# Performance work log

Measured on AMD Instinct MI355X. Metric: run time of the kernel, lower is better.

Reference implementation:

```python
import jax, jax.numpy as jnp
import numpy as np

VOCAB, HIDDEN = 32000, 512
BATCH, SEQLEN = 256, 128


def setup_inputs() -> dict:
    key = jax.random.key(0)
    k1, k2, k3, k4, k5 = jax.random.split(key, 5)
    bound = 1.0 / np.sqrt(HIDDEN)  # PyTorch RNNCell init scale
    return {
        "input": jax.random.randint(k1, (BATCH, SEQLEN), 0, VOCAB, dtype=jnp.int64),
        "hidden": jnp.zeros((BATCH, HIDDEN), dtype=jnp.float32),
        "emb_table": jax.random.normal(k2, (VOCAB, HIDDEN), dtype=jnp.float32),
        "W_ih": jax.random.uniform(k3, (HIDDEN, HIDDEN), jnp.float32, -bound, bound),
        "W_hh": jax.random.uniform(k4, (HIDDEN, HIDDEN), jnp.float32, -bound, bound),
        "b_ih": jax.random.uniform(k5, (HIDDEN,), jnp.float32, -bound, bound),
        "b_hh": jax.random.uniform(jax.random.fold_in(key, 9), (HIDDEN,), jnp.float32, -bound, bound),
    }


def reference(input, hidden, emb_table, W_ih, W_hh, b_ih, b_hh):
    # embedded: [B, T, H]
    embedded = emb_table[input]
    # Precompute the input projection for all timesteps in one GEMM: [B, T, H]
    x_proj = jnp.einsum("bth,ih->bti", embedded, W_ih) + b_ih

    def step(h, x_t):
        # PyTorch RNNCell: h' = tanh(x W_ih^T + b_ih + h W_hh^T + b_hh)
        h_new = jnp.tanh(x_t + h @ W_hh.T + b_hh)
        return h_new, h_new

    h_final, outs = jax.lax.scan(step, hidden, jnp.swapaxes(x_proj, 0, 1))
    outputs = jnp.swapaxes(outs, 0, 1)  # [B, T, H]
    return outputs, h_final
```

## Files before the change

kernel.cpp:

```cpp
#include <hip/hip_runtime.h>
#include <cstdint>

#define VOCAB   32000
#define HIDDEN  512
#define BATCH   256
#define SEQLEN  128

typedef _Float16 f16;
typedef _Float16 f16x2 __attribute__((ext_vector_type(2)));
typedef _Float16 f16x4 __attribute__((ext_vector_type(4)));
typedef _Float16 f16x8 __attribute__((ext_vector_type(8)));
typedef float    f32x4 __attribute__((ext_vector_type(4)));


__global__ __launch_bounds__(256) void conv_f16_kernel(
    const float* __restrict__ emb, const float* __restrict__ wih,
    const float* __restrict__ whh, f16* __restrict__ emb16,
    f16* __restrict__ wih16, f16* __restrict__ whh16)
{
  const long long EMB_N = (long long)VOCAB * HIDDEN;
  const long long W_N   = (long long)HIDDEN * HIDDEN;
  long long idx = ((long long)blockIdx.x * blockDim.x + threadIdx.x) * 4;
  const float* src; f16* dst; long long off;
  if (idx < EMB_N)            { src = emb; dst = emb16; off = idx; }
  else if (idx < EMB_N + W_N) { src = wih; dst = wih16; off = idx - EMB_N; }
  else                        { src = whh; dst = whh16; off = idx - EMB_N - W_N; }
  float4 v = *(const float4*)(src + off);
  f16x4 o = { (f16)v.x, (f16)v.y, (f16)v.z, (f16)v.w };
  *(f16x4*)(dst + off) = o;
}

__global__ __launch_bounds__(256) void xproj_kernel(
    const int*   __restrict__ tokens,
    const f16*   __restrict__ emb16,
    const f16*   __restrict__ wih16,
    const float* __restrict__ b_ih,
    float*       __restrict__ out)
{
  const int lane = threadIdx.x & 63;
  const int wave = threadIdx.x >> 6;
  const int m0 = blockIdx.y * 128 + (wave >> 1) * 64;
  const int n0 = blockIdx.x * 128 + (wave & 1) * 64;
  const int lr = lane & 15;
  const int lg = lane >> 4;

  const f16* aptr[4];
  const f16* bptr[4];
#pragma unroll
  for (int mi = 0; mi < 4; ++mi) {
    int row = m0 + mi * 16 + lr;
    int tok = tokens[row];
    aptr[mi] = emb16 + (long long)tok * HIDDEN;
  }
#pragma unroll
  for (int ni = 0; ni < 4; ++ni) {
    int col = n0 + ni * 16 + lr;
    bptr[ni] = wih16 + (long long)col * HIDDEN;
  }

  f32x4 acc[4][4];
#pragma unroll
  for (int ni = 0; ni < 4; ++ni) {
    float b = b_ih[n0 + ni * 16 + lr];
#pragma unroll
    for (int mi = 0; mi < 4; ++mi) acc[mi][ni] = (f32x4){b, b, b, b};
  }

  for (int kt = 0; kt < 16; ++kt) {
    const int kb = kt * 32 + lg * 8;
    f16x8 af[4], bf[4];
#pragma unroll
    for (int mi = 0; mi < 4; ++mi) af[mi] = *(const f16x8*)(aptr[mi] + kb);
#pragma unroll
    for (int ni = 0; ni < 4; ++ni) bf[ni] = *(const f16x8*)(bptr[ni] + kb);
#pragma unroll
    for (int mi = 0; mi < 4; ++mi)
#pragma unroll
      for (int ni = 0; ni < 4; ++ni)
        acc[mi][ni] = __builtin_amdgcn_mfma_f32_16x16x32_f16(
            af[mi], bf[ni], acc[mi][ni], 0, 0, 0);
  }

#pragma unroll
  for (int mi = 0; mi < 4; ++mi)
#pragma unroll
    for (int ni = 0; ni < 4; ++ni)
#pragma unroll
      for (int j = 0; j < 4; ++j) {
        int rg = m0 + mi * 16 + lg * 4 + j;
        int cg = n0 + ni * 16 + lr;
        out[(long long)rg * HIDDEN + cg] = acc[mi][ni][j];
      }
}

__device__ __forceinline__ float dp2(uint32_t w, uint32_t h, float acc) {
  f16x2 wv = __builtin_bit_cast(f16x2, w);
  f16x2 hv = __builtin_bit_cast(f16x2, h);
#if __has_builtin(__builtin_amdgcn_fdot2)
  return __builtin_amdgcn_fdot2(wv, hv, acc, false);
#else
  acc = fmaf((float)wv.x, (float)hv.x, acc);
  acc = fmaf((float)wv.y, (float)hv.y, acc);
  return acc;
#endif
}

__global__ __launch_bounds__(1024) void rnn_kernel(
    const f16*   __restrict__ whh16,
    const float* __restrict__ b_hh,
    const float* __restrict__ h0,
    float*       __restrict__ out,
    float*       __restrict__ hfin)
{
  extern __shared__ char smem[];
  uint4* hh4  = (uint4*)smem;
  float* pacc = (float*)(smem + 1024);
  uint4* ldsW = (uint4*)(smem + 1024 + 4096);

  const int tid = threadIdx.x;
  const int q   = tid >> 9;
  const int i   = tid & 511;
  const int b   = blockIdx.x;

  const uint4* wrow = (const uint4*)(whh16 + ((long long)i * HIDDEN + q * 256));
  uint32_t wreg[96];
#pragma unroll
  for (int c = 0; c < 24; ++c) {
    uint4 v = wrow[c];
    wreg[4 * c + 0] = v.x; wreg[4 * c + 1] = v.y;
    wreg[4 * c + 2] = v.z; wreg[4 * c + 3] = v.w;
  }
#pragma unroll
  for (int c = 0; c < 8; ++c) ldsW[c * 1024 + tid] = wrow[24 + c];

  if (q == 0) ((f16*)hh4)[i] = (f16)h0[(long long)b * HIDDEN + i];
  const float bh = b_hh[i];
  __syncthreads();

  float* xprow = out + (long long)b * SEQLEN * HIDDEN;
  float xpn = xprow[i];

  for (int t = 0; t < SEQLEN; ++t) {
    const float xpv = xpn;
    const int tn = (t < SEQLEN - 1) ? t + 1 : t;
    xpn = xprow[tn * HIDDEN + i];

    float a0 = 0.f, a1 = 0.f, a2 = 0.f, a3 = 0.f;
#pragma unroll
    for (int c = 0; c < 24; ++c) {
      uint4 hv = hh4[q * 32 + c];
      a0 = dp2(wreg[4 * c + 0], hv.x, a0);
      a1 = dp2(wreg[4 * c + 1], hv.y, a1);
      a2 = dp2(wreg[4 * c + 2], hv.z, a2);
      a3 = dp2(wreg[4 * c + 3], hv.w, a3);
    }
#pragma unroll
    for (int c = 0; c < 8; ++c) {
      uint4 hv = hh4[q * 32 + 24 + c];
      uint4 wv = ldsW[c * 1024 + tid];
      a0 = dp2(wv.x, hv.x, a0);
      a1 = dp2(wv.y, hv.y, a1);
      a2 = dp2(wv.z, hv.z, a2);
      a3 = dp2(wv.w, hv.w, a3);
    }
    pacc[tid] = (a0 + a1) + (a2 + a3);
    __syncthreads();

    if (q == 0) {
      float pre = xpv + bh + pacc[i] + pacc[i + 512];
      float h = tanhf(pre);
      xprow[t * HIDDEN + i] = h;
      ((f16*)hh4)[i] = (f16)h;
      if (t == SEQLEN - 1) hfin[(long long)b * HIDDEN + i] = h;
    }
    __syncthreads();
  }
}

extern "C" void kernel_launch(void* const* d_in, const int* in_sizes, int n_in,
                              void* d_out, int out_size, void* d_ws, size_t ws_size,
                              hipStream_t stream) {
  const int*   tokens = (const int*)  d_in[0];
  const float* hidden = (const float*)d_in[1];
  const float* emb    = (const float*)d_in[2];
  const float* wih    = (const float*)d_in[3];
  const float* whh    = (const float*)d_in[4];
  const float* bih    = (const float*)d_in[5];
  const float* bhh    = (const float*)d_in[6];
  float* out = (float*)d_out;

  f16* emb16 = (f16*)d_ws;
  f16* wih16 = (f16*)((char*)d_ws + 32768000);
  f16* whh16 = (f16*)((char*)d_ws + 33292288);

  conv_f16_kernel<<<16512, 256, 0, stream>>>(emb, wih, whh, emb16, wih16, whh16);

  xproj_kernel<<<dim3(4, 256), 256, 0, stream>>>(tokens, emb16, wih16, bih, out);

  const int LDSB = 1024 + 4096 + 131072;
  hipFuncSetAttribute((const void*)rnn_kernel,
                      hipFuncAttributeMaxDynamicSharedMemorySize, LDSB);
  rnn_kernel<<<BATCH, 1024, LDSB, stream>>>(
      whh16, bhh, hidden, out, out + (long long)BATCH * SEQLEN * HIDDEN);
}
```

Before: 417.3 us.

## Split RNN recurrence across 8 k-slices with 4 rows per thread

Restructures the per-step matvec so each thread handles 4 output rows over a 64-wide k-slice instead of one row over a 256-wide half. Each loaded h vector chunk is now reused across 4 rows, which cuts LDS reads of h per dot product. The cost is a larger partial-sum buffer and an 8-way reduction per output. Launch bounds now also carry a min-blocks hint.

```diff
diff --git a/kernel.cpp b/kernel.cpp
--- a/kernel.cpp
+++ b/kernel.cpp
@@ -105,7 +105,7 @@
 #endif
 }
 
-__global__ __launch_bounds__(1024) void rnn_kernel(
+__global__ __launch_bounds__(1024, 4) void rnn_kernel(
     const f16*   __restrict__ whh16,
     const float* __restrict__ b_hh,
     const float* __restrict__ h0,
@@ -115,63 +115,79 @@
   extern __shared__ char smem[];
   uint4* hh4  = (uint4*)smem;
   float* pacc = (float*)(smem + 1024);
-  uint4* ldsW = (uint4*)(smem + 1024 + 4096);
+  uint4* ldsW = (uint4*)(smem + 1024 + 16384);
 
   const int tid = threadIdx.x;
-  const int q   = tid >> 9;
-  const int i   = tid & 511;
+  const int w   = tid >> 6;
+  const int l   = tid & 63;
+  const int s   = w >> 1;
+  const int ib  = (w & 1) * 64 + l;
   const int b   = blockIdx.x;
 
-  const uint4* wrow = (const uint4*)(whh16 + ((long long)i * HIDDEN + q * 256));
   uint32_t wreg[96];
 #pragma unroll
-  for (int c = 0; c < 24; ++c) {
-    uint4 v = wrow[c];
-    wreg[4 * c + 0] = v.x; wreg[4 * c + 1] = v.y;
-    wreg[4 * c + 2] = v.z; wreg[4 * c + 3] = v.w;
-  }
-#pragma unroll
-  for (int c = 0; c < 8; ++c) ldsW[c * 1024 + tid] = wrow[24 + c];
-
-  if (q == 0) ((f16*)hh4)[i] = (f16)h0[(long long)b * HIDDEN + i];
-  const float bh = b_hh[i];
+  for (int o = 0; o < 3; ++o) {
+    const uint4* wr = (const uint4*)(whh16 + ((long long)(ib + o * 128) * HIDDEN + s * 64));
+#pragma unroll
+    for (int c = 0; c < 8; ++c) {
+      uint4 v = wr[c];
+      wreg[o * 32 + c * 4 + 0] = v.x; wreg[o * 32 + c * 4 + 1] = v.y;
+      wreg[o * 32 + c * 4 + 2] = v.z; wreg[o * 32 + c * 4 + 3] = v.w;
+    }
+  }
+  {
+    const uint4* wr3 = (const uint4*)(whh16 + ((long long)(ib + 384) * HIDDEN + s * 64));
+#pragma unroll
+    for (int c = 0; c < 8; ++c) ldsW[c * 1024 + tid] = wr3[c];
+  }
+
+  if (tid < 512) ((f16*)hh4)[tid] = (f16)h0[(long long)b * HIDDEN + tid];
+  const float bh = (tid < 512) ? b_hh[tid] : 0.f;
+  float* xprow = out + (long long)b * SEQLEN * HIDDEN;
+  float xpn = (tid < 512) ? xprow[tid] : 0.f;
   __syncthreads();
-
-  float* xprow = out + (long long)b * SEQLEN * HIDDEN;
-  float xpn = xprow[i];
 
   for (int t = 0; t < SEQLEN; ++t) {
     const float xpv = xpn;
     const int tn = (t < SEQLEN - 1) ? t + 1 : t;
-    xpn = xprow[tn * HIDDEN + i];
+    if (tid < 512) xpn = xprow[tn * HIDDEN + tid];
 
     float a0 = 0.f, a1 = 0.f, a2 = 0.f, a3 = 0.f;
 #pragma unroll
-    for (int c = 0; c < 24; ++c) {
-      uint4 hv = hh4[q * 32 + c];
-      a0 = dp2(wreg[4 * c + 0], hv.x, a0);
-      a1 = dp2(wreg[4 * c + 1], hv.y, a1);
-      a2 = dp2(wreg[4 * c + 2], hv.z, a2);
-      a3 = dp2(wreg[4 * c + 3], hv.w, a3);
+    for (int hc = 0; hc < 8; ++hc) {
+      uint4 hv = hh4[s * 8 + hc];
+      uint4 w3 = ldsW[hc * 1024 + tid];
+      a0 = dp2(wreg[0 * 32 + hc * 4 + 0], hv.x, a0);
+      a0 = dp2(wreg[0 * 32 + hc * 4 + 1], hv.y, a0);
+      a0 = dp2(wreg[0 * 32 + hc * 4 + 2], hv.z, a0);
+      a0 = dp2(wreg[0 * 32 + hc * 4 + 3], hv.w, a0);
+      a1 = dp2(wreg[1 * 32 + hc * 4 + 0], hv.x, a1);
+      a1 = dp2(wreg[1 * 32 + hc * 4 + 1], hv.y, a1);
+      a1 = dp2(wreg[1 * 32 + hc * 4 + 2], hv.z, a1);
+      a1 = dp2(wreg[1 * 32 + hc * 4 + 3], hv.w, a1);
+      a2 = dp2(wreg[2 * 32 + hc * 4 + 0], hv.x, a2);
+      a2 = dp2(wreg[2 * 32 + hc * 4 + 1], hv.y, a2);
+      a2 = dp2(wreg[2 * 32 + hc * 4 + 2], hv.z, a2);
+      a2 = dp2(wreg[2 * 32 + hc * 4 + 3], hv.w, a2);
+      a3 = dp2(w3.x, hv.x, a3);
+      a3 = dp2(w3.y, hv.y, a3);
+      a3 = dp2(w3.z, hv.z, a3);
+      a3 = dp2(w3.w, hv.w, a3);
     }
-#pragma unroll
-    for (int c = 0; c < 8; ++c) {
-      uint4 hv = hh4[q * 32 + 24 + c];
-      uint4 wv = ldsW[c * 1024 + tid];
-      a0 = dp2(wv.x, hv.x, a0);
-      a1 = dp2(wv.y, hv.y, a1);
-      a2 = dp2(wv.z, hv.z, a2);
-      a3 = dp2(wv.w, hv.w, a3);
-    }
-    pacc[tid] = (a0 + a1) + (a2 + a3);
+    pacc[s * 512 + ib]       = a0;
+    pacc[s * 512 + ib + 128] = a1;
+    pacc[s * 512 + ib + 256] = a2;
+    pacc[s * 512 + ib + 384] = a3;
     __syncthreads();
 
-    if (q == 0) {
-      float pre = xpv + bh + pacc[i] + pacc[i + 512];
+    if (tid < 512) {
+      float pre = xpv + bh;
+#pragma unroll
+      for (int s2 = 0; s2 < 8; ++s2) pre += pacc[s2 * 512 + tid];
       float h = tanhf(pre);
-      xprow[t * HIDDEN + i] = h;
-      ((f16*)hh4)[i] = (f16)h;
-      if (t == SEQLEN - 1) hfin[(long long)b * HIDDEN + i] = h;
+      xprow[t * HIDDEN + tid] = h;
+      ((f16*)hh4)[tid] = (f16)h;
+      if (t == SEQLEN - 1) hfin[(long long)b * HIDDEN + tid] = h;
     }
     __syncthreads();
   }
@@ -197,7 +213,7 @@
 
   xproj_kernel<<<dim3(4, 256), 256, 0, stream>>>(tokens, emb16, wih16, bih, out);
 
-  const int LDSB = 1024 + 4096 + 131072;
+  const int LDSB = 1024 + 16384 + 131072;
   hipFuncSetAttribute((const void*)rnn_kernel,
                       hipFuncAttributeMaxDynamicSharedMemorySize, LDSB);
   rnn_kernel<<<BATCH, 1024, LDSB, stream>>>(
```

New measurement: 399.2 us. 4.3% less time.
